# Performance work log

Measured on AMD Instinct MI355X. Metric: run time of the kernel, lower is better.

The kernel has to match this reference:

```python
import jax, jax.numpy as jnp
import numpy as np

EMBED_DIM = 1024
NUM_HEADS = 16
D_K = EMBED_DIM // NUM_HEADS


def setup_inputs() -> dict:
    key = jax.random.key(0)
    ks = jax.random.split(key, 5)
    s = 1.0 / np.sqrt(EMBED_DIM)  # roughly match nn.Linear init scale
    return {
        "x": jax.random.normal(ks[0], (2, 2048, EMBED_DIM), dtype=jnp.float32),
        "wq": jax.random.normal(ks[1], (EMBED_DIM, EMBED_DIM), dtype=jnp.float32) * s,
        "wk": jax.random.normal(ks[2], (EMBED_DIM, EMBED_DIM), dtype=jnp.float32) * s,
        "wv": jax.random.normal(ks[3], (EMBED_DIM, EMBED_DIM), dtype=jnp.float32) * s,
        "wo": jax.random.normal(ks[4], (EMBED_DIM, EMBED_DIM), dtype=jnp.float32) * s,
    }


def reference(x, wq, wk, wv, wo):
    b, s, e = x.shape
    # nn.Linear(bias=False): y = x @ W.T
    def split_heads(t):
        return t.reshape(b, s, NUM_HEADS, D_K).transpose(0, 2, 1, 3)  # [b,h,s,d]
    q = split_heads(x @ wq.T)
    k = split_heads(x @ wk.T)
    v = split_heads(x @ wv.T)
    scores = jnp.einsum("bhqd,bhkd->bhqk", q, k) / jnp.sqrt(jnp.float32(D_K))
    attn = jax.nn.softmax(scores, axis=-1)
    out = jnp.einsum("bhqk,bhkd->bhqd", attn, v)  # [b,h,s,d]
    out = out.transpose(0, 2, 1, 3).reshape(b, s, e)
    return out @ wo.T
```

## Files before the change

kernel.cpp:

```cpp
#include <hip/hip_runtime.h>
#include <stdint.h>

typedef unsigned short u16;
typedef float f32x4 __attribute__((ext_vector_type(4)));
typedef __bf16 bf16x8 __attribute__((ext_vector_type(8)));
typedef short s16x4 __attribute__((ext_vector_type(4)));

__device__ __forceinline__ u16 f2bf(float f) {
  union { float f; uint32_t u; } c; c.f = f;
  uint32_t u = c.u;
  u += 0x7fffu + ((u >> 16) & 1u);
  return (u16)(u >> 16);
}

__device__ __forceinline__ uint32_t pkbf(float a, float b) {
  union { float f; uint32_t u; } ua, ub; ua.f = a; ub.f = b;
  return __builtin_amdgcn_perm(ub.u, ua.u, 0x07060302u);
}

#define GLOAD_LDS16(g, l)                                                              \
  __builtin_amdgcn_global_load_lds((__attribute__((address_space(1))) void*)(g),       \
                                   (__attribute__((address_space(3))) void*)(l), 16, 0, 0)

__global__ __launch_bounds__(256) void cvt_all(const float* __restrict__ x,
                                               const float* __restrict__ wq,
                                               const float* __restrict__ wk,
                                               const float* __restrict__ wv,
                                               const float* __restrict__ wo,
                                               u16* __restrict__ xb,
                                               u16* __restrict__ wqkvb,
                                               u16* __restrict__ wob) {
  int bx = blockIdx.x;
  const float* src;
  u16* dst;
  int i;
  if (bx < 4096) {
    src = x; dst = xb; i = bx * 256 + threadIdx.x;
  } else {
    int r = bx - 4096;
    int w = r >> 10;
    i = (r & 1023) * 256 + threadIdx.x;
    if (w == 0)      { src = wq; dst = wqkvb; }
    else if (w == 1) { src = wk; dst = wqkvb + 1048576; }
    else if (w == 2) { src = wv; dst = wqkvb + 2097152; }
    else             { src = wo; dst = wob; }
  }
  const float4 v = ((const float4*)src)[i];
  ushort4 o;
  o.x = f2bf(v.x); o.y = f2bf(v.y); o.z = f2bf(v.z); o.w = f2bf(v.w);
  ((ushort4*)dst)[i] = o;
}

__global__ __launch_bounds__(256, 3) void gemm_qkv(const u16* __restrict__ A,
                                                   const u16* __restrict__ B,
                                                   u16* __restrict__ QKb,
                                                   u16* __restrict__ Vt) {
  const int K = 1024;
  __shared__ __align__(16) u16 sA[3 * 4096];
  __shared__ __align__(16) u16 sB[3 * 4096];
  const int tid = threadIdx.x;
  const int lane = tid & 63;
  const int wave = tid >> 6;
  const int quad = lane >> 4, l16 = lane & 15;
  const int wm = (wave >> 1) * 64, wn = (wave & 1) * 64;
  const int bm = blockIdx.y * 128, bn = blockIdx.x * 128;

  f32x4 acc[4][4];
#pragma unroll
  for (int i = 0; i < 4; i++)
#pragma unroll
    for (int j = 0; j < 4; j++) acc[i][j] = (f32x4){0.f, 0.f, 0.f, 0.f};

#define QKV_STAGE(t, bi)                                                           \
  {                                                                                \
    const int k0s = (t) * 32;                                                      \
    char* dA = (char*)(sA + (bi) * 4096);                                          \
    char* dB = (char*)(sB + (bi) * 4096);                                          \
    _Pragma("unroll")                                                              \
    for (int k2 = 0; k2 < 2; k2++) {                                               \
      int u = k2 * 256 + tid;                                                      \
      int row = u >> 2, c4 = (u & 3) ^ (row & 3);                                  \
      GLOAD_LDS16(A + (size_t)(bm + row) * K + k0s + c4 * 8, dA + u * 16);         \
      GLOAD_LDS16(B + (size_t)(bn + row) * K + k0s + c4 * 8, dB + u * 16);         \
    }                                                                              \
  }

  QKV_STAGE(0, 0);
  QKV_STAGE(1, 1);

  int cur = 0, stg = 2;
  for (int T = 0; T < 32; ++T) {
    if (T < 31) asm volatile("s_waitcnt vmcnt(4)" ::: "memory");
    else        asm volatile("s_waitcnt vmcnt(0)" ::: "memory");
    __builtin_amdgcn_s_barrier();
    asm volatile("" ::: "memory");
    if (T < 30) QKV_STAGE(T + 2, stg);

    const u16* cA = sA + cur * 4096;
    const u16* cB = sB + cur * 4096;
    bf16x8 af[4], bfr[4];
#pragma unroll
    for (int mt = 0; mt < 4; mt++) {
      int ra = wm + mt * 16 + l16;
      af[mt] = *(const bf16x8*)&cA[ra * 32 + ((quad ^ (ra & 3)) * 8)];
    }
#pragma unroll
    for (int nt = 0; nt < 4; nt++) {
      int rb = wn + nt * 16 + l16;
      bfr[nt] = *(const bf16x8*)&cB[rb * 32 + ((quad ^ (rb & 3)) * 8)];
    }
#pragma unroll
    for (int mt = 0; mt < 4; mt++)
#pragma unroll
      for (int nt = 0; nt < 4; nt++)
        acc[mt][nt] = __builtin_amdgcn_mfma_f32_16x16x32_bf16(af[mt], bfr[nt], acc[mt][nt], 0, 0, 0);

    cur = (cur == 2) ? 0 : cur + 1;
    stg = (stg == 2) ? 0 : stg + 1;
  }
#undef QKV_STAGE

  if (blockIdx.x < 16) {
    const float qs = (blockIdx.x < 8) ? 0.18033688011f : 1.0f;
#pragma unroll
    for (int mt = 0; mt < 4; mt++)
#pragma unroll
      for (int nt = 0; nt < 4; nt++)
#pragma unroll
        for (int r = 0; r < 4; r++) {
          int row = bm + wm + mt * 16 + quad * 4 + r;
          int col = bn + wn + nt * 16 + l16;
          QKb[(size_t)row * 2048 + col] = f2bf(acc[mt][nt][r] * qs);
        }
  } else {
#pragma unroll
    for (int mt = 0; mt < 4; mt++)
#pragma unroll
      for (int nt = 0; nt < 4; nt++) {
        int hd = (bn - 2048) + wn + nt * 16 + l16;
        int tok = bm + wm + mt * 16 + quad * 4;
        ushort4 o;
        o.x = f2bf(acc[mt][nt][0]);
        o.y = f2bf(acc[mt][nt][1]);
        o.z = f2bf(acc[mt][nt][2]);
        o.w = f2bf(acc[mt][nt][3]);
        *(ushort4*)&Vt[(size_t)hd * 4096 + tok] = o;
      }
  }
}

__global__ __launch_bounds__(512, 4) void attn_fwd(const u16* __restrict__ QKb,
                                                   const u16* __restrict__ Vt,
                                                   u16* __restrict__ O) {
  const int bx = blockIdx.x;
  const int qt = bx >> 5;
  const int h  = (bx >> 1) & 15;
  const int b  = bx & 1;
  const int tid = threadIdx.x;
  const int lane = tid & 63;
  const int wave = tid >> 6;
  const int wq = wave >> 1;
  const int wk = wave & 1;
  const int quad = lane >> 4, l16 = lane & 15;

  __shared__ __align__(16) u16 smem[36864];
  u16* sQ = smem;
  u16* sK = smem + 8192;
  u16* sV = smem + 20480;

  const int tok0 = b * 2048;
  const int q0 = qt * 128;
  const int colh = h * 64;

#pragma unroll
  for (int k2 = 0; k2 < 2; k2++) {
    int c = k2 * 512 + tid;
    int row = c >> 3, c8 = (c & 7) ^ (row & 7);
    GLOAD_LDS16(QKb + (size_t)(tok0 + q0 + row) * 2048 + colh + c8 * 8,
                (char*)sQ + c * 16);
  }
#pragma unroll
  for (int t = 0; t < 2; t++) {
    int c = tid;
    int row = c >> 3, c8 = (c & 7) ^ (row & 7);
    GLOAD_LDS16(QKb + (size_t)(tok0 + t * 64 + row) * 2048 + 1024 + colh + c8 * 8,
                (char*)(sK + t * 4096) + c * 16);
    GLOAD_LDS16(Vt + (size_t)(colh + row) * 4096 + tok0 + t * 64 + c8 * 8,
                (char*)(sV + t * 4096) + c * 16);
  }
  asm volatile("s_waitcnt vmcnt(4)" ::: "memory");
  __builtin_amdgcn_s_barrier();
  asm volatile("" ::: "memory");

  bf16x8 aq[2][2];
#pragma unroll
  for (int sub = 0; sub < 2; sub++)
#pragma unroll
    for (int kh = 0; kh < 2; kh++) {
      int rq = wq * 32 + sub * 16 + l16;
      aq[sub][kh] = *(const bf16x8*)&sQ[rq * 64 + (((kh * 4 + quad) ^ (rq & 7)) * 8)];
    }

  f32x4 oacc[2][4];
  float lsum[2];
#pragma unroll
  for (int sub = 0; sub < 2; sub++) {
    lsum[sub] = 0.f;
#pragma unroll
    for (int db = 0; db < 4; db++) oacc[sub][db] = (f32x4){0.f, 0.f, 0.f, 0.f};
  }

  int kc = 0, stg3 = 2;

#define ITER_LOAD(IT, SS)                                                            \
  {                                                                                  \
    asm volatile("s_waitcnt lgkmcnt(0)" ::: "memory");                               \
    if ((IT) < 31) asm volatile("s_waitcnt vmcnt(2)" ::: "memory");                  \
    else           asm volatile("s_waitcnt vmcnt(0)" ::: "memory");                  \
    __builtin_amdgcn_s_barrier();                                                    \
    asm volatile("" ::: "memory");                                                   \
    if ((IT) < 30) {                                                                 \
      const int nkv = ((IT) + 2) * 64;                                               \
      int c = tid;                                                                   \
      int row = c >> 3, c8 = (c & 7) ^ (row & 7);                                    \
      GLOAD_LDS16(QKb + (size_t)(tok0 + nkv + row) * 2048 + 1024 + colh + c8 * 8,    \
                  (char*)(sK + stg3 * 4096) + c * 16);                               \
      GLOAD_LDS16(Vt + (size_t)(colh + row) * 4096 + tok0 + nkv + c8 * 8,            \
                  (char*)(sV + (((IT) + 2) & 3) * 4096) + c * 16);                   \
    }                                                                                \
    const u16* sKc = sK + kc * 4096;                                                 \
    bf16x8 kf[2][2];                                                                 \
    _Pragma("unroll")                                                                \
    for (int nt = 0; nt < 2; nt++)                                                   \
      _Pragma("unroll")                                                              \
      for (int kh = 0; kh < 2; kh++) {                                               \
        int rr = wk * 32 + nt * 16 + l16;                                            \
        kf[nt][kh] = *(const bf16x8*)&sKc[rr * 64 + (((kh * 4 + quad) ^ (rr & 7)) * 8)]; \
      }                                                                              \
    _Pragma("unroll")                                                                \
    for (int sub = 0; sub < 2; sub++)                                                \
      _Pragma("unroll")                                                              \
      for (int nt = 0; nt < 2; nt++) {                                               \
        f32x4 c0 = (f32x4){0.f, 0.f, 0.f, 0.f};                                      \
        c0 = __builtin_amdgcn_mfma_f32_16x16x32_bf16(kf[nt][0], aq[sub][0], c0, 0, 0, 0); \
        SS[sub][nt] = __builtin_amdgcn_mfma_f32_16x16x32_bf16(kf[nt][1], aq[sub][1], c0, 0, 0, 0); \
      }                                                                              \
    kc = (kc == 2) ? 0 : kc + 1;                                                     \
    stg3 = (stg3 == 2) ? 0 : stg3 + 1;                                               \
  }

#define ITER_SOFT(TT, SS)                                                            \
  {                                                                                  \
    const u16* sVp = sV + ((TT) & 3) * 4096;                                         \
    _Pragma("unroll")                                                                \
    for (int nt = 0; nt < 2; nt++) {                                                 \
      s16x4 vf[4];                                                                   \
      _Pragma("unroll")                                                              \
      for (int db = 0; db < 4; db++) {                                               \
        int row = db * 16 + l16;                                                     \
        int c16 = ((wk * 2 + nt) * 2 + (quad >> 1)) ^ (row & 7);                     \
        vf[db] = *(const s16x4*)&sVp[row * 64 + c16 * 8 + (quad & 1) * 4];           \
      }                                                                              \
      _Pragma("unroll")                                                              \
      for (int sub = 0; sub < 2; sub++) {                                            \
        f32x4 cS = SS[sub][nt];                                                      \
        float e0 = __builtin_amdgcn_exp2f(cS[0]);                                    \
        float e1 = __builtin_amdgcn_exp2f(cS[1]);                                    \
        float e2 = __builtin_amdgcn_exp2f(cS[2]);                                    \
        float e3 = __builtin_amdgcn_exp2f(cS[3]);                                    \
        lsum[sub] += (e0 + e1) + (e2 + e3);                                          \
        union { uint32_t u[2]; s16x4 v; } bb;                                        \
        bb.u[0] = pkbf(e0, e1);                                                      \
        bb.u[1] = pkbf(e2, e3);                                                      \
        _Pragma("unroll")                                                            \
        for (int db = 0; db < 4; db++)                                               \
          oacc[sub][db] = __builtin_amdgcn_mfma_f32_16x16x16bf16_1k(vf[db], bb.v, oacc[sub][db], 0, 0, 0); \
      }                                                                              \
    }                                                                                \
  }

  f32x4 SA[2][2], SB[2][2];
  ITER_LOAD(0, SA);
  for (int it = 1; it < 31; it += 2) {
    ITER_LOAD(it, SB);
    ITER_SOFT(it - 1, SA);
    ITER_LOAD(it + 1, SA);
    ITER_SOFT(it, SB);
  }
  ITER_LOAD(31, SB);
  ITER_SOFT(30, SA);
  ITER_SOFT(31, SB);
#undef ITER_LOAD
#undef ITER_SOFT

  asm volatile("s_waitcnt lgkmcnt(0)" ::: "memory");
  __builtin_amdgcn_s_barrier();

#pragma unroll
  for (int sub = 0; sub < 2; sub++) {
    float v = lsum[sub];
    v += __shfl_xor(v, 16, 64);
    v += __shfl_xor(v, 32, 64);
    lsum[sub] = v;
  }

  float* Rbase = (float*)smem + wq * 2048;
  float* lsumT = (float*)((char*)smem + 32768);

  if (wk == 0) {
#pragma unroll
    for (int sub = 0; sub < 2; sub++) {
#pragma unroll
      for (int db = 0; db < 4; db++) {
        int q = sub * 16 + l16;
        int d = db * 16 + quad * 4;
        *(f32x4*)&Rbase[q * 64 + (d ^ ((q & 7) << 3))] = oacc[sub][db];
      }
      if (quad == 0) lsumT[wq * 32 + sub * 16 + l16] = lsum[sub];
    }
  }
  __builtin_amdgcn_s_barrier();
  if (wk == 1) {
#pragma unroll
    for (int sub = 0; sub < 2; sub++) {
      int q = sub * 16 + l16;
      float rt = 1.0f / (lsum[sub] + lsumT[wq * 32 + q]);
#pragma unroll
      for (int db = 0; db < 4; db++) {
        int d = db * 16 + quad * 4;
        f32x4 o = *(const f32x4*)&Rbase[q * 64 + (d ^ ((q & 7) << 3))] + oacc[sub][db];
        ushort4 st;
        st.x = f2bf(o[0] * rt);
        st.y = f2bf(o[1] * rt);
        st.z = f2bf(o[2] * rt);
        st.w = f2bf(o[3] * rt);
        *(ushort4*)&O[(size_t)(tok0 + q0 + wq * 32 + q) * 1024 + colh + d] = st;
      }
    }
  }
}

__global__ __launch_bounds__(256) void gemm_out(const u16* __restrict__ A,
                                                const u16* __restrict__ B,
                                                float* __restrict__ C) {
  const int N = 1024, K = 1024;
  __shared__ __align__(16) u16 sA[3 * 4096];
  __shared__ __align__(16) u16 sB[3 * 2048];
  const int tid = threadIdx.x;
  const int lane = tid & 63;
  const int wave = tid >> 6;
  const int quad = lane >> 4, l16 = lane & 15;
  const int wm = (wave >> 1) * 64, wn = (wave & 1) * 32;
  const int bm = blockIdx.y * 128, bn = blockIdx.x * 64;

  f32x4 acc[4][2];
#pragma unroll
  for (int i = 0; i < 4; i++)
#pragma unroll
    for (int j = 0; j < 2; j++) acc[i][j] = (f32x4){0.f, 0.f, 0.f, 0.f};

#define OUT_STAGE(t, bi)                                                           \
  {                                                                                \
    const int k0s = (t) * 32;                                                      \
    char* dA = (char*)(sA + (bi) * 4096);                                          \
    char* dB = (char*)(sB + (bi) * 2048);                                          \
    _Pragma("unroll")                                                              \
    for (int k2 = 0; k2 < 2; k2++) {                                               \
      int u = k2 * 256 + tid;                                                      \
      int row = u >> 2, c4 = (u & 3) ^ (row & 3);                                  \
      GLOAD_LDS16(A + (size_t)(bm + row) * K + k0s + c4 * 8, dA + u * 16);         \
    }                                                                              \
    {                                                                              \
      int u = tid;                                                                 \
      int row = u >> 2, c4 = (u & 3) ^ (row & 3);                                  \
      GLOAD_LDS16(B + (size_t)(bn + row) * K + k0s + c4 * 8, dB + u * 16);         \
    }                                                                              \
  }

  OUT_STAGE(0, 0);
  OUT_STAGE(1, 1);

  int cur = 0, stg = 2;
  for (int T = 0; T < 32; ++T) {
    if (T < 31) asm volatile("s_waitcnt vmcnt(3)" ::: "memory");
    else        asm volatile("s_waitcnt vmcnt(0)" ::: "memory");
    __builtin_amdgcn_s_barrier();
    asm volatile("" ::: "memory");
    if (T < 30) OUT_STAGE(T + 2, stg);

    const u16* cA = sA + cur * 4096;
    const u16* cB = sB + cur * 2048;
    bf16x8 af[4], bfr[2];
#pragma unroll
    for (int mt = 0; mt < 4; mt++) {
      int ra = wm + mt * 16 + l16;
      af[mt] = *(const bf16x8*)&cA[ra * 32 + ((quad ^ (ra & 3)) * 8)];
    }
#pragma unroll
    for (int nt = 0; nt < 2; nt++) {
      int rb = wn + nt * 16 + l16;
      bfr[nt] = *(const bf16x8*)&cB[rb * 32 + ((quad ^ (rb & 3)) * 8)];
    }
#pragma unroll
    for (int mt = 0; mt < 4; mt++)
#pragma unroll
      for (int nt = 0; nt < 2; nt++)
        acc[mt][nt] = __builtin_amdgcn_mfma_f32_16x16x32_bf16(af[mt], bfr[nt], acc[mt][nt], 0, 0, 0);

    cur = (cur == 2) ? 0 : cur + 1;
    stg = (stg == 2) ? 0 : stg + 1;
  }
#undef OUT_STAGE

#pragma unroll
  for (int mt = 0; mt < 4; mt++)
#pragma unroll
    for (int nt = 0; nt < 2; nt++)
#pragma unroll
      for (int r = 0; r < 4; r++) {
        int row = bm + wm + mt * 16 + quad * 4 + r;
        int col = bn + wn + nt * 16 + l16;
        C[(size_t)row * N + col] = acc[mt][nt][r];
      }
}

extern "C" void kernel_launch(void* const* d_in, const int* in_sizes, int n_in,
                              void* d_out, int out_size, void* d_ws, size_t ws_size,
                              hipStream_t stream) {
  const float* x  = (const float*)d_in[0];
  const float* wq = (const float*)d_in[1];
  const float* wk = (const float*)d_in[2];
  const float* wv = (const float*)d_in[3];
  const float* wo = (const float*)d_in[4];
  float* out = (float*)d_out;
  char* ws = (char*)d_ws;
  const size_t MB = 1u << 20;

  u16* xb    = (u16*)(ws);
  u16* wqkvb = (u16*)(ws + 8 * MB);
  u16* wob   = (u16*)(ws + 14 * MB);
  u16* QKb   = (u16*)(ws + 16 * MB);
  u16* Vtb   = (u16*)(ws + 32 * MB);
  u16* Ob    = xb;

  cvt_all<<<8192, 256, 0, stream>>>(x, wq, wk, wv, wo, xb, wqkvb, wob);

  gemm_qkv<<<dim3(24, 32), 256, 0, stream>>>(xb, wqkvb, QKb, Vtb);

  attn_fwd<<<512, 512, 0, stream>>>(QKb, Vtb, Ob);

  gemm_out<<<dim3(16, 32), 256, 0, stream>>>(Ob, wob, out);
}
```

Baseline: 179.8 us.

## Switch QKV and output GEMMs to BK=64 double-buffered pipeline, widen out tile

Both bf16 GEMMs move from a 3-stage pipeline with a K-step of 32 to a 2-stage double buffer with a K-step of 64 and an 8-way XOR swizzle, which halves the number of barriers and loop iterations. The output projection also grows its tile from 128x64 to 128x128, so the grid drops to 256 blocks and each block reuses its A tile across more columns. In exchange there is less prefetch depth, a full vmcnt(0) wait at the end of each iteration, more LDS per block (occupancy bounded at 2 blocks), and fewer blocks than CUs for gemm_out.

After: 184.9 us. 2.9% more time.

```diff
diff --git a/kernel.cpp b/kernel.cpp
--- a/kernel.cpp
+++ b/kernel.cpp
@@ -51,13 +51,13 @@
   ((ushort4*)dst)[i] = o;
 }
 
-__global__ __launch_bounds__(256, 3) void gemm_qkv(const u16* __restrict__ A,
+__global__ __launch_bounds__(256, 2) void gemm_qkv(const u16* __restrict__ A,
                                                    const u16* __restrict__ B,
                                                    u16* __restrict__ QKb,
                                                    u16* __restrict__ Vt) {
   const int K = 1024;
-  __shared__ __align__(16) u16 sA[3 * 4096];
-  __shared__ __align__(16) u16 sB[3 * 4096];
+  __shared__ __align__(16) u16 sA[2 * 8192];
+  __shared__ __align__(16) u16 sB[2 * 8192];
   const int tid = threadIdx.x;
   const int lane = tid & 63;
   const int wave = tid >> 6;
@@ -73,50 +73,49 @@
 
 #define QKV_STAGE(t, bi)                                                           \
   {                                                                                \
-    const int k0s = (t) * 32;                                                      \
-    char* dA = (char*)(sA + (bi) * 4096);                                          \
-    char* dB = (char*)(sB + (bi) * 4096);                                          \
+    const int k0s = (t) * 64;                                                      \
+    char* dA = (char*)(sA + (bi) * 8192);                                          \
+    char* dB = (char*)(sB + (bi) * 8192);                                          \
     _Pragma("unroll")                                                              \
-    for (int k2 = 0; k2 < 2; k2++) {                                               \
+    for (int k2 = 0; k2 < 4; k2++) {                                               \
       int u = k2 * 256 + tid;                                                      \
-      int row = u >> 2, c4 = (u & 3) ^ (row & 3);                                  \
-      GLOAD_LDS16(A + (size_t)(bm + row) * K + k0s + c4 * 8, dA + u * 16);         \
-      GLOAD_LDS16(B + (size_t)(bn + row) * K + k0s + c4 * 8, dB + u * 16);         \
+      int row = u >> 3, c8 = (u & 7) ^ (row & 7);                                  \
+      GLOAD_LDS16(A + (size_t)(bm + row) * K + k0s + c8 * 8, dA + u * 16);         \
+      GLOAD_LDS16(B + (size_t)(bn + row) * K + k0s + c8 * 8, dB + u * 16);         \
     }                                                                              \
   }
 
   QKV_STAGE(0, 0);
-  QKV_STAGE(1, 1);
-
-  int cur = 0, stg = 2;
-  for (int T = 0; T < 32; ++T) {
-    if (T < 31) asm volatile("s_waitcnt vmcnt(4)" ::: "memory");
-    else        asm volatile("s_waitcnt vmcnt(0)" ::: "memory");
+  asm volatile("s_waitcnt vmcnt(0)" ::: "memory");
+  __builtin_amdgcn_s_barrier();
+  asm volatile("" ::: "memory");
+
+  for (int T = 0; T < 16; ++T) {
+    const int cur = T & 1;
+    if (T < 15) QKV_STAGE(T + 1, cur ^ 1);
+
+    const u16* cA = sA + cur * 8192;
+    const u16* cB = sB + cur * 8192;
+    bf16x8 af[4][2], bfr[4][2];
+#pragma unroll
+    for (int mt = 0; mt < 4; mt++)
+#pragma unroll
+      for (int kh = 0; kh < 2; kh++) {
+        int ra = wm + mt * 16 + l16;
+        af[mt][kh] = *(const bf16x8*)&cA[ra * 64 + (((kh * 4 + quad) ^ (ra & 7)) * 8)];
+        int rb = wn + mt * 16 + l16;
+        bfr[mt][kh] = *(const bf16x8*)&cB[rb * 64 + (((kh * 4 + quad) ^ (rb & 7)) * 8)];
+      }
+#pragma unroll
+    for (int mt = 0; mt < 4; mt++)
+#pragma unroll
+      for (int nt = 0; nt < 4; nt++) {
+        acc[mt][nt] = __builtin_amdgcn_mfma_f32_16x16x32_bf16(af[mt][0], bfr[nt][0], acc[mt][nt], 0, 0, 0);
+        acc[mt][nt] = __builtin_amdgcn_mfma_f32_16x16x32_bf16(af[mt][1], bfr[nt][1], acc[mt][nt], 0, 0, 0);
+      }
+    asm volatile("s_waitcnt vmcnt(0)" ::: "memory");
     __builtin_amdgcn_s_barrier();
     asm volatile("" ::: "memory");
-    if (T < 30) QKV_STAGE(T + 2, stg);
-
-    const u16* cA = sA + cur * 4096;
-    const u16* cB = sB + cur * 4096;
-    bf16x8 af[4], bfr[4];
-#pragma unroll
-    for (int mt = 0; mt < 4; mt++) {
-      int ra = wm + mt * 16 + l16;
-      af[mt] = *(const bf16x8*)&cA[ra * 32 + ((quad ^ (ra & 3)) * 8)];
-    }
-#pragma unroll
-    for (int nt = 0; nt < 4; nt++) {
-      int rb = wn + nt * 16 + l16;
-      bfr[nt] = *(const bf16x8*)&cB[rb * 32 + ((quad ^ (rb & 3)) * 8)];
-    }
-#pragma unroll
-    for (int mt = 0; mt < 4; mt++)
-#pragma unroll
-      for (int nt = 0; nt < 4; nt++)
-        acc[mt][nt] = __builtin_amdgcn_mfma_f32_16x16x32_bf16(af[mt], bfr[nt], acc[mt][nt], 0, 0, 0);
-
-    cur = (cur == 2) ? 0 : cur + 1;
-    stg = (stg == 2) ? 0 : stg + 1;
   }
 #undef QKV_STAGE
 
@@ -340,82 +339,77 @@
   }
 }
 
-__global__ __launch_bounds__(256) void gemm_out(const u16* __restrict__ A,
-                                                const u16* __restrict__ B,
-                                                float* __restrict__ C) {
+__global__ __launch_bounds__(256, 2) void gemm_out(const u16* __restrict__ A,
+                                                   const u16* __restrict__ B,
+                                                   float* __restrict__ C) {
   const int N = 1024, K = 1024;
-  __shared__ __align__(16) u16 sA[3 * 4096];
-  __shared__ __align__(16) u16 sB[3 * 2048];
+  __shared__ __align__(16) u16 sA[2 * 8192];
+  __shared__ __align__(16) u16 sB[2 * 8192];
   const int tid = threadIdx.x;
   const int lane = tid & 63;
   const int wave = tid >> 6;
   const int quad = lane >> 4, l16 = lane & 15;
-  const int wm = (wave >> 1) * 64, wn = (wave & 1) * 32;
-  const int bm = blockIdx.y * 128, bn = blockIdx.x * 64;
-
-  f32x4 acc[4][2];
+  const int wm = (wave >> 1) * 64, wn = (wave & 1) * 64;
+  const int bm = blockIdx.y * 128, bn = blockIdx.x * 128;
+
+  f32x4 acc[4][4];
 #pragma unroll
   for (int i = 0; i < 4; i++)
 #pragma unroll
-    for (int j = 0; j < 2; j++) acc[i][j] = (f32x4){0.f, 0.f, 0.f, 0.f};
+    for (int j = 0; j < 4; j++) acc[i][j] = (f32x4){0.f, 0.f, 0.f, 0.f};
 
 #define OUT_STAGE(t, bi)                                                           \
   {                                                                                \
-    const int k0s = (t) * 32;                                                      \
-    char* dA = (char*)(sA + (bi) * 4096);                                          \
-    char* dB = (char*)(sB + (bi) * 2048);                                          \
+    const int k0s = (t) * 64;                                                      \
+    char* dA = (char*)(sA + (bi) * 8192);                                          \
+    char* dB = (char*)(sB + (bi) * 8192);                                          \
     _Pragma("unroll")                                                              \
-    for (int k2 = 0; k2 < 2; k2++) {                                               \
+    for (int k2 = 0; k2 < 4; k2++) {                                               \
       int u = k2 * 256 + tid;                                                      \
-      int row = u >> 2, c4 = (u & 3) ^ (row & 3);                                  \
-      GLOAD_LDS16(A + (size_t)(bm + row) * K + k0s + c4 * 8, dA + u * 16);         \
+      int row = u >> 3, c8 = (u & 7) ^ (row & 7);                                  \
+      GLOAD_LDS16(A + (size_t)(bm + row) * K + k0s + c8 * 8, dA + u * 16);         \
+      GLOAD_LDS16(B + (size_t)(bn + row) * K + k0s + c8 * 8, dB + u * 16);         \
     }                                                                              \
-    {                                                                              \
-      int u = tid;                                                                 \
-      int row = u >> 2, c4 = (u & 3) ^ (row & 3);                                  \
-      GLOAD_LDS16(B + (size_t)(bn + row) * K + k0s + c4 * 8, dB + u * 16);         \
-    }                                                                              \
   }
 
   OUT_STAGE(0, 0);
-  OUT_STAGE(1, 1);
-
-  int cur = 0, stg = 2;
-  for (int T = 0; T < 32; ++T) {
-    if (T < 31) asm volatile("s_waitcnt vmcnt(3)" ::: "memory");
-    else        asm volatile("s_waitcnt vmcnt(0)" ::: "memory");
+  asm volatile("s_waitcnt vmcnt(0)" ::: "memory");
+  __builtin_amdgcn_s_barrier();
+  asm volatile("" ::: "memory");
+
+  for (int T = 0; T < 16; ++T) {
+    const int cur = T & 1;
+    if (T < 15) OUT_STAGE(T + 1, cur ^ 1);
+
+    const u16* cA = sA + cur * 8192;
+    const u16* cB = sB + cur * 8192;
+    bf16x8 af[4][2], bfr[4][2];
+#pragma unroll
+    for (int mt = 0; mt < 4; mt++)
+#pragma unroll
+      for (int kh = 0; kh < 2; kh++) {
+        int ra = wm + mt * 16 + l16;
+        af[mt][kh] = *(const bf16x8*)&cA[ra * 64 + (((kh * 4 + quad) ^ (ra & 7)) * 8)];
+        int rb = wn + mt * 16 + l16;
+        bfr[mt][kh] = *(const bf16x8*)&cB[rb * 64 + (((kh * 4 + quad) ^ (rb & 7)) * 8)];
+      }
+#pragma unroll
+    for (int mt = 0; mt < 4; mt++)
+#pragma unroll
+      for (int nt = 0; nt < 4; nt++) {
+        acc[mt][nt] = __builtin_amdgcn_mfma_f32_16x16x32_bf16(af[mt][0], bfr[nt][0], acc[mt][nt], 0, 0, 0);
+        acc[mt][nt] = __builtin_amdgcn_mfma_f32_16x16x32_bf16(af[mt][1], bfr[nt][1], acc[mt][nt], 0, 0, 0);
+      }
+    asm volatile("s_waitcnt vmcnt(0)" ::: "memory");
     __builtin_amdgcn_s_barrier();
     asm volatile("" ::: "memory");
-    if (T < 30) OUT_STAGE(T + 2, stg);
-
-    const u16* cA = sA + cur * 4096;
-    const u16* cB = sB + cur * 2048;
-    bf16x8 af[4], bfr[2];
-#pragma unroll
-    for (int mt = 0; mt < 4; mt++) {
-      int ra = wm + mt * 16 + l16;
-      af[mt] = *(const bf16x8*)&cA[ra * 32 + ((quad ^ (ra & 3)) * 8)];
-    }
-#pragma unroll
-    for (int nt = 0; nt < 2; nt++) {
-      int rb = wn + nt * 16 + l16;
-      bfr[nt] = *(const bf16x8*)&cB[rb * 32 + ((quad ^ (rb & 3)) * 8)];
-    }
-#pragma unroll
-    for (int mt = 0; mt < 4; mt++)
-#pragma unroll
-      for (int nt = 0; nt < 2; nt++)
-        acc[mt][nt] = __builtin_amdgcn_mfma_f32_16x16x32_bf16(af[mt], bfr[nt], acc[mt][nt], 0, 0, 0);
-
-    cur = (cur == 2) ? 0 : cur + 1;
-    stg = (stg == 2) ? 0 : stg + 1;
   }
 #undef OUT_STAGE
 
 #pragma unroll
   for (int mt = 0; mt < 4; mt++)
 #pragma unroll
-    for (int nt = 0; nt < 2; nt++)
+    for (int nt = 0; nt < 4; nt++)
 #pragma unroll
       for (int r = 0; r < 4; r++) {
         int row = bm + wm + mt * 16 + quad * 4 + r;
@@ -449,5 +443,5 @@
 
   attn_fwd<<<512, 512, 0, stream>>>(QKb, Vtb, Ob);
 
-  gemm_out<<<dim3(16, 32), 256, 0, stream>>>(Ob, wob, out);
-}
+  gemm_out<<<dim3(8, 32), 256, 0, stream>>>(Ob, wob, out);
+}
```
